# Performance work log

Hardware: AMD Instinct MI355X
Metric: run time of the kernel (lower is better)

The kernel has to match this reference:

```python
import jax, jax.numpy as jnp
import numpy as np

PAD_IDX = 0
EPS = 1e-5


def make_pos(L):
    # phrase[i, j] = j - i, i.e. row i is range(-i, L-i)
    phrase = (np.arange(L)[None, :] - np.arange(L)[:, None]).astype(np.float32)
    half = int(np.ceil(L / 2))
    freq = np.linspace(0.0, L, L, dtype=np.float32)[1:half]          # [F]
    pos = freq[:, None, None] * phrase[None] / L * 2.0 * np.pi       # [F, L, L]
    pos = np.concatenate([np.cos(pos), np.sin(pos)], axis=0)        # [2F, L, L]
    return jnp.asarray(np.transpose(pos, (1, 0, 2)))                # [L, P=2F, L]


def setup_inputs() -> dict:
    key = jax.random.key(0)
    ks = jax.random.split(key, 8)
    B, L, V, D, H = 2048, 64, 4096, 64, 8
    P = 2 * (int(np.ceil(L / 2)) - 1)  # 62
    inputs = jax.random.randint(ks[0], (B, L), 0, V)
    W_emb = jax.random.normal(ks[1], (V, D), jnp.float32) * 0.02
    W_emb = W_emb.at[PAD_IDX].set(0.0)  # padding_idx row is zero
    W_qkv = jax.random.normal(ks[2], (3 * H * D, D), jnp.float32) * 0.02
    W_pos = jax.random.normal(ks[3], (P, L), jnp.float32) * 0.02
    ln_g = jnp.ones((D,), jnp.float32)
    ln_b = jnp.zeros((D,), jnp.float32)
    W1 = jax.random.normal(ks[4], (64, H), jnp.float32) * 0.1
    b1 = jnp.zeros((64,), jnp.float32)
    W2 = jax.random.normal(ks[5], (32, 64), jnp.float32) * 0.1
    b2 = jnp.zeros((32,), jnp.float32)
    return dict(inputs=inputs, W_emb=W_emb, W_qkv=W_qkv, W_pos=W_pos,
                ln_g=ln_g, ln_b=ln_b, W1=W1, b1=b1, W2=W2, b2=b2,
                n_words=4, n_names=16)


def reference(inputs, W_emb, W_qkv, W_pos, ln_g, ln_b, W1, b1, W2, b2, n_words, n_names):
    B, L = inputs.shape
    V, D = W_emb.shape
    H = W_qkv.shape[0] // (3 * D)
    pos = make_pos(L)  # [L, P, L]
    P = pos.shape[1]

    # compute_qkv: per-char q/k/v tables, then gather per token.
    qkv = (W_emb @ W_qkv.T).reshape(V, 3 * H, D)
    q, k, v = qkv[:, :H], qkv[:, H:2 * H], qkv[:, 2 * H:]
    q_t = jnp.take(q, inputs, axis=0)  # [B, L, H, D]
    k_t = jnp.take(k, inputs, axis=0)
    v_t = jnp.take(v, inputs, axis=0)

    # Equivalent to gathering char_sim[h, ids, ids]: qkv is a per-token linear,
    # so q[ids] @ k[ids]^T == char_sim.index_select(1, ids).index_select(-1, ids).
    sim = jnp.einsum('blhd,bmhd->bhlm', q_t, k_t) / jnp.sqrt(jnp.float32(D))
    key_pad = (inputs == PAD_IDX)[:, None, None, :]
    sim = jnp.where(key_pad, jnp.float32(-1e9), sim)  # char_sim[:, :, pad_idx] = -1e9

    # positional bias: Linear(L->P) on clipped scores, contracted with pos basis.
    sim_clip = jnp.where(sim > -1e8, sim, jnp.float32(0.0))
    pos_w = jnp.einsum('bhlm,pm->bhlp', sim_clip, W_pos)        # [B, H, L, P]
    pos_bias = jnp.einsum('bhlp,lpm->bhlm', pos_w, pos) / P     # mean over P

    attn = jax.nn.softmax(sim + pos_bias, axis=-1)              # dropout p=0 -> id
    out = jnp.einsum('bhlm,bmhd->blhd', attn, v_t)              # [B, L, H, D]

    # sdpa LayerNorm over word_vec_d
    mu = out.mean(-1, keepdims=True)
    var = out.var(-1, keepdims=True)
    out = (out - mu) * jax.lax.rsqrt(var + EPS) * ln_g + ln_b

    # MLP over the head dimension: [B, L, D, H] -> [B, L, D, 32]
    ft = jnp.swapaxes(out, 2, 3)
    h1 = jax.nn.relu(jnp.einsum('bldh,oh->bldo', ft, W1) + b1)
    h2 = jnp.einsum('bldo,po->bldp', h1, W2) + b2
    char_ft = h2.reshape(B, L, -1)                              # [B, L, D*32]

    # masked mean pooling over chars -> word feature
    maskf = (inputs != PAD_IDX).astype(char_ft.dtype)
    word_ft = jnp.einsum('bl,blf->bf', maskf, char_ft) / maskf.sum(-1, keepdims=True)

    # equal-size splits: words -> names (mean) -> groups of names
    Fdim = word_ft.shape[-1]
    name_ft = word_ft.reshape(B // n_words, n_words, Fdim).mean(1)
    return name_ft.reshape(-1, n_names, Fdim)
```

## Files before the change

### kernel.cpp

```cpp
#include <hip/hip_runtime.h>
#include <hip/hip_bf16.h>


typedef __attribute__((ext_vector_type(8))) short short8;
typedef __attribute__((ext_vector_type(4))) float f32x4;

union FragU { uint4 u; short8 v; };

__device__ __forceinline__ unsigned short f2bf(float f) {
    union { float f; unsigned int i; } c; c.f = f;
    unsigned int i = c.i;
    unsigned int r = (i + 0x7fffu + ((i >> 16) & 1u)) >> 16;
    return (unsigned short)r;
}
__device__ __forceinline__ float asf(unsigned int u) {
    union { unsigned int i; float f; } c; c.i = u; return c.f;
}
__device__ __forceinline__ float bfsel(uint2 g, int i) {
    unsigned u = (i < 2) ? g.x : g.y;
    return asf((i & 1) ? (u & 0xffff0000u) : (u << 16));
}

__device__ __forceinline__ void packstore4(unsigned* rowptr, int c,
                                           float v0, float v1, float v2, float v3) {
    float p0 = __shfl_xor(v0, 1), p1 = __shfl_xor(v1, 1);
    float p2 = __shfl_xor(v2, 1), p3 = __shfl_xor(v3, 1);
    int odd = c & 1;
    unsigned a0 = odd ? ((unsigned)f2bf(p2) | ((unsigned)f2bf(v2) << 16))
                      : ((unsigned)f2bf(v0) | ((unsigned)f2bf(p0) << 16));
    unsigned a1 = odd ? ((unsigned)f2bf(p3) | ((unsigned)f2bf(v3) << 16))
                      : ((unsigned)f2bf(v1) | ((unsigned)f2bf(p1) << 16));
    int ba = (c >> 1) + (odd ? 16 : 0);
    rowptr[ba] = a0; rowptr[ba + 8] = a1;
}

__global__ __launch_bounds__(256) void k_qkv(const float* __restrict__ W_emb,
                                             const float* __restrict__ W_qkv,
                                             unsigned short* __restrict__ qkvb) {
    __shared__ float At[4096];
    __shared__ float Bt[4096];
    int t = threadIdx.x;
    int bt = blockIdx.x / 24, rt = blockIdx.x - bt * 24;
    int r = t >> 2, part = t & 3;
    const float4* esrc = (const float4*)(W_emb + (size_t)((bt << 6) + r) * 64 + part * 16);
    const float4* wsrc = (const float4*)(W_qkv + (size_t)((rt << 6) + r) * 64 + part * 16);
#pragma unroll
    for (int j = 0; j < 4; ++j) {
        float4 e4 = esrc[j], w4 = wsrc[j];
        int c0 = part * 16 + j * 4;
        At[(c0 + 0) * 64 + r] = e4.x; At[(c0 + 1) * 64 + r] = e4.y;
        At[(c0 + 2) * 64 + r] = e4.z; At[(c0 + 3) * 64 + r] = e4.w;
        Bt[(c0 + 0) * 64 + r] = w4.x; Bt[(c0 + 1) * 64 + r] = w4.y;
        Bt[(c0 + 2) * 64 + r] = w4.z; Bt[(c0 + 3) * 64 + r] = w4.w;
    }
    __syncthreads();
    int l0 = (t >> 4) << 2, m0 = (t & 15) << 2;
    float acc[4][4] = {};
#pragma unroll 4
    for (int k = 0; k < 64; ++k) {
        float4 a  = *(const float4*)(At + k * 64 + l0);
        float4 bb = *(const float4*)(Bt + k * 64 + m0);
        float aa[4] = {a.x, a.y, a.z, a.w};
        float bv[4] = {bb.x, bb.y, bb.z, bb.w};
#pragma unroll
        for (int i = 0; i < 4; ++i)
#pragma unroll
            for (int j = 0; j < 4; ++j)
                acc[i][j] = fmaf(aa[i], bv[j], acc[i][j]);
    }
#pragma unroll
    for (int i = 0; i < 4; ++i) {
        unsigned w0 = (unsigned)f2bf(acc[i][0]) | ((unsigned)f2bf(acc[i][1]) << 16);
        unsigned w1 = (unsigned)f2bf(acc[i][2]) | ((unsigned)f2bf(acc[i][3]) << 16);
        unsigned* dst = (unsigned*)(qkvb + (size_t)((bt << 6) + l0 + i) * 1536 + (rt << 6) + m0);
        dst[0] = w0; dst[1] = w1;
    }
}

__global__ void k_tab(const float* __restrict__ W_pos,
                      unsigned short* __restrict__ cst,
                      unsigned short* __restrict__ csl,
                      unsigned short* __restrict__ wpos) {
    int t = threadIdx.x;
    const float w = 6.283185307179586f / 63.0f;
    for (int e = t; e < 4096; e += 256) {
        int row = e >> 6, col = e & 63;
        {
            int j = col, x = row;
            float val = 0.0f;
            if (j < 31)       val = cosf(w * (float)(((j + 1) * x) % 63));
            else if (j >= 32 && j < 63) val = sinf(w * (float)(((j - 31) * x) % 63));
            cst[e] = f2bf(val);
        }
        {
            int j = row, x = col;
            float val = 0.0f;
            if (j < 31)       val = cosf(w * (float)(((j + 1) * x) % 63));
            else if (j >= 32 && j < 63) val = sinf(w * (float)(((j - 31) * x) % 63));
            csl[e] = f2bf(val);
        }
        {
            int j = row;
            float val = 0.0f;
            if (j < 31) val = W_pos[j * 64 + col];
            else if (j >= 32 && j < 63) val = W_pos[(j - 1) * 64 + col];
            wpos[e] = f2bf(val);
        }
    }
}

__global__ __launch_bounds__(128, 4) void k_attn(
    const int* __restrict__ inputs,
    const unsigned short* __restrict__ qkvb,
    const unsigned short* __restrict__ cstg,
    const unsigned short* __restrict__ cslg,
    const unsigned short* __restrict__ wposg,
    const float* __restrict__ ln_g,
    const float* __restrict__ ln_b,
    unsigned short* __restrict__ out_n)
{
    __shared__ __align__(16) unsigned int smem[4608];
    unsigned int* S0d = smem;
    unsigned int* S1d = smem + 2304;
    int t = threadIdx.x, w2 = t >> 6, lane = t & 63;
    int b = blockIdx.x >> 3, h = blockIdx.x & 7;
    const int* toks = inputs + b * 64;
    int r = lane & 15, q = lane >> 4, c = r;
    int tk = toks[lane];
    int mt0 = 2 * w2;

    int mk[4]; float gvv[4], bvv[4];
#pragma unroll
    for (int nt = 0; nt < 4; ++nt) {
        mk[nt] = (toks[16 * nt + c] == 0);
        gvv[nt] = ln_g[16 * nt + c];
        bvv[nt] = ln_b[16 * nt + c];
    }

    {
        const uint4* src = (const uint4*)(qkvb + (size_t)tk * 1536 + (w2 ? 512 : 0) + h * 64);
        uint4* dst = (uint4*)((w2 ? S1d : S0d) + lane * 36);
#pragma unroll
        for (int j = 0; j < 8; ++j) dst[j] = src[j];
    }
    __syncthreads();

    f32x4 sc[2][4], acc[2][4];
    const f32x4 zf = {0.f, 0.f, 0.f, 0.f};

#pragma unroll
    for (int u = 0; u < 2; ++u)
#pragma unroll
        for (int nt = 0; nt < 4; ++nt) sc[u][nt] = zf;
#pragma unroll
    for (int ks = 0; ks < 2; ++ks) {
        FragU Af[2], Bf[4];
#pragma unroll
        for (int u = 0; u < 2; ++u)
            Af[u].u = *(const uint4*)(S0d + (16 * (mt0 + u) + r) * 36 + 16 * ks + 4 * q);
#pragma unroll
        for (int nt = 0; nt < 4; ++nt)
            Bf[nt].u = *(const uint4*)(S1d + (16 * nt + r) * 36 + 16 * ks + 4 * q);
#pragma unroll
        for (int u = 0; u < 2; ++u)
#pragma unroll
            for (int nt = 0; nt < 4; ++nt)
                sc[u][nt] = __builtin_amdgcn_mfma_f32_16x16x32_bf16(Af[u].v, Bf[nt].v, sc[u][nt], 0, 0, 0);
    }
#pragma unroll
    for (int u = 0; u < 2; ++u) {
#pragma unroll
        for (int nt = 0; nt < 4; ++nt) {
            f32x4 vv = sc[u][nt];
#pragma unroll
            for (int i = 0; i < 4; ++i) vv[i] = mk[nt] ? 0.0f : vv[i] * 0.125f;
            sc[u][nt] = vv;
        }
#pragma unroll
        for (int i = 0; i < 4; ++i) {
            int l = 16 * (mt0 + u) + 4 * q + i;
            packstore4(S0d + l * 36, c, sc[u][0][i], sc[u][1][i], sc[u][2][i], sc[u][3][i]);
        }
    }
    __syncthreads();

#pragma unroll
    for (int u = 0; u < 2; ++u)
#pragma unroll
        for (int nt = 0; nt < 4; ++nt) acc[u][nt] = zf;
#pragma unroll
    for (int ks = 0; ks < 2; ++ks) {
        FragU Af[2], Bf[4];
#pragma unroll
        for (int u = 0; u < 2; ++u)
            Af[u].u = *(const uint4*)(S0d + (16 * (mt0 + u) + r) * 36 + 16 * ks + 4 * q);
#pragma unroll
        for (int nt = 0; nt < 4; ++nt)
            Bf[nt].u = *(const uint4*)(wposg + (16 * nt + r) * 64 + 32 * ks + 8 * q);
#pragma unroll
        for (int u = 0; u < 2; ++u)
#pragma unroll
            for (int nt = 0; nt < 4; ++nt)
                acc[u][nt] = __builtin_amdgcn_mfma_f32_16x16x32_bf16(Af[u].v, Bf[nt].v, acc[u][nt], 0, 0, 0);
    }
#pragma unroll
    for (int u = 0; u < 2; ++u) {
        int mt = mt0 + u;
        uint2 t00 = *(const uint2*)(cslg + (c) * 64 + 16 * mt + 4 * q);
        uint2 t01 = *(const uint2*)(cslg + (32 + c) * 64 + 16 * mt + 4 * q);
        uint2 t10 = *(const uint2*)(cslg + (16 + c) * 64 + 16 * mt + 4 * q);
        uint2 t11 = *(const uint2*)(cslg + (48 + c) * 64 + 16 * mt + 4 * q);
#pragma unroll
        for (int i = 0; i < 4; ++i) {
            int l = 16 * mt + 4 * q + i;
            float cv0 = bfsel(t00, i), sv0 = bfsel(t01, i);
            float cv1 = bfsel(t10, i), sv1 = bfsel(t11, i);
            float pc0 = acc[u][0][i], ps0 = acc[u][2][i];
            float pc1 = acc[u][1][i], ps1 = acc[u][3][i];
            float u0 = pc0 * cv0 - ps0 * sv0;
            float u1 = pc1 * cv1 - ps1 * sv1;
            float u2 = pc0 * sv0 + ps0 * cv0;
            float u3 = pc1 * sv1 + ps1 * cv1;
            packstore4(S1d + l * 36, c, u0, u1, u2, u3);
        }
    }

#pragma unroll
    for (int u = 0; u < 2; ++u)
#pragma unroll
        for (int nt = 0; nt < 4; ++nt) acc[u][nt] = zf;
#pragma unroll
    for (int ks = 0; ks < 2; ++ks) {
        FragU Af[2], Bf[4];
#pragma unroll
        for (int u = 0; u < 2; ++u)
            Af[u].u = *(const uint4*)(S1d + (16 * (mt0 + u) + r) * 36 + 16 * ks + 4 * q);
#pragma unroll
        for (int nt = 0; nt < 4; ++nt)
            Bf[nt].u = *(const uint4*)(cstg + (16 * nt + r) * 64 + 32 * ks + 8 * q);
#pragma unroll
        for (int u = 0; u < 2; ++u)
#pragma unroll
            for (int nt = 0; nt < 4; ++nt)
                acc[u][nt] = __builtin_amdgcn_mfma_f32_16x16x32_bf16(Af[u].v, Bf[nt].v, acc[u][nt], 0, 0, 0);
    }

    uint4 V4[4];
    {
        const uint4* vsrc = (const uint4*)(qkvb + (size_t)tk * 1536 + 1024 + h * 64 + 32 * w2);
#pragma unroll
        for (int j = 0; j < 4; ++j) V4[j] = vsrc[j];
    }

#pragma unroll
    for (int u = 0; u < 2; ++u)
#pragma unroll
        for (int i = 0; i < 4; ++i) {
            int l = 16 * (mt0 + u) + 4 * q + i;
            float e0 = mk[0] ? 0.f : __expf(fmaf(acc[u][0][i], 1.0f / 62.0f, sc[u][0][i]));
            float e1 = mk[1] ? 0.f : __expf(fmaf(acc[u][1][i], 1.0f / 62.0f, sc[u][1][i]));
            float e2 = mk[2] ? 0.f : __expf(fmaf(acc[u][2][i], 1.0f / 62.0f, sc[u][2][i]));
            float e3 = mk[3] ? 0.f : __expf(fmaf(acc[u][3][i], 1.0f / 62.0f, sc[u][3][i]));
            float s = e0 + e1 + e2 + e3;
            s += __shfl_xor(s, 1);
            s += __shfl_xor(s, 2);
            s += __shfl_xor(s, 4);
            s += __shfl_xor(s, 8);
            float inv = 1.0f / s;
            packstore4(S0d + l * 36, c, e0 * inv, e1 * inv, e2 * inv, e3 * inv);
        }

    {
        int odd = lane & 1;
        const unsigned* Vd = (const unsigned*)V4;
#pragma unroll
        for (int jj = 0; jj < 16; ++jj) {
            unsigned my = Vd[jj];
            unsigned pr = __shfl_xor(my, 1);
            unsigned val = odd ? ((pr >> 16) | (my & 0xffff0000u))
                               : ((my & 0xffffu) | (pr << 16));
            S1d[(32 * w2 + 2 * jj + odd) * 36 + (lane >> 1)] = val;
        }
    }
    __syncthreads();

#pragma unroll
    for (int u = 0; u < 2; ++u)
#pragma unroll
        for (int nt = 0; nt < 4; ++nt) acc[u][nt] = zf;
#pragma unroll
    for (int ks = 0; ks < 2; ++ks) {
        FragU Af[2], Bf[4];
#pragma unroll
        for (int u = 0; u < 2; ++u)
            Af[u].u = *(const uint4*)(S0d + (16 * (mt0 + u) + r) * 36 + 16 * ks + 4 * q);
#pragma unroll
        for (int nt = 0; nt < 4; ++nt)
            Bf[nt].u = *(const uint4*)(S1d + (16 * nt + r) * 36 + 16 * ks + 4 * q);
#pragma unroll
        for (int u = 0; u < 2; ++u)
#pragma unroll
            for (int nt = 0; nt < 4; ++nt)
                acc[u][nt] = __builtin_amdgcn_mfma_f32_16x16x32_bf16(Af[u].v, Bf[nt].v, acc[u][nt], 0, 0, 0);
    }
    {
        unsigned* outw = (unsigned*)out_n;
        size_t hb = ((size_t)b * 8 + h) * 64;
#pragma unroll
        for (int u = 0; u < 2; ++u)
#pragma unroll
            for (int i = 0; i < 4; ++i) {
                int l = 16 * (mt0 + u) + 4 * q + i;
                float v0 = acc[u][0][i], v1 = acc[u][1][i], v2 = acc[u][2][i], v3 = acc[u][3][i];
                float s1 = v0 + v1 + v2 + v3;
                float s2 = v0 * v0 + v1 * v1 + v2 * v2 + v3 * v3;
                s1 += __shfl_xor(s1, 1); s2 += __shfl_xor(s2, 1);
                s1 += __shfl_xor(s1, 2); s2 += __shfl_xor(s2, 2);
                s1 += __shfl_xor(s1, 4); s2 += __shfl_xor(s2, 4);
                s1 += __shfl_xor(s1, 8); s2 += __shfl_xor(s2, 8);
                float mu = s1 * (1.0f / 64.0f);
                float var = s2 * (1.0f / 64.0f) - mu * mu;
                float rstd = rsqrtf(var + 1e-5f);
                float y0 = (v0 - mu) * rstd * gvv[0] + bvv[0];
                float y1 = (v1 - mu) * rstd * gvv[1] + bvv[1];
                float y2 = (v2 - mu) * rstd * gvv[2] + bvv[2];
                float y3 = (v3 - mu) * rstd * gvv[3] + bvv[3];
                packstore4(outw + (hb + l) * 32, c, y0, y1, y2, y3);
            }
    }
}

__global__ __launch_bounds__(256) void k_mlp(const int* __restrict__ inputs,
                                             const unsigned short* __restrict__ out_n,
                                             const float* __restrict__ W1,
                                             const float* __restrict__ b1,
                                             float* __restrict__ gws) {
    __shared__ unsigned short XT[8320];
    __shared__ float wl[64];
    int t = threadIdx.x, w = t >> 6, lane = t & 63;
    int b = blockIdx.x;
    int ot = w >> 1, dt = w & 1;
    int kq = lane >> 4, n = lane & 15;

    if (t < 64) {
        int tok = inputs[b * 64 + t];
        unsigned long long bal = __ballot(tok != 0);
        int cnt = __popcll(bal);
        if (cnt < 1) cnt = 1;
        wl[t] = (tok != 0) ? 1.0f / (float)cnt : 0.0f;
    }

    FragU Wf[2];
    float b1v[2];
#pragma unroll
    for (int om = 0; om < 2; ++om) {
        int o = 32 * ot + 16 * om + n;
        b1v[om] = b1[o];
        if (kq == 0) {
            const float4* wsrc = (const float4*)(W1 + o * 8);
            float4 wa = wsrc[0], wb = wsrc[1];
            Wf[om].u.x = (unsigned)f2bf(wa.x) | ((unsigned)f2bf(wa.y) << 16);
            Wf[om].u.y = (unsigned)f2bf(wa.z) | ((unsigned)f2bf(wa.w) << 16);
            Wf[om].u.z = (unsigned)f2bf(wb.x) | ((unsigned)f2bf(wb.y) << 16);
            Wf[om].u.w = (unsigned)f2bf(wb.z) | ((unsigned)f2bf(wb.w) << 16);
        } else {
            Wf[om].u = make_uint4(0, 0, 0, 0);
        }
    }

    f32x4 racc[2][2];
    const f32x4 zf = {0.f, 0.f, 0.f, 0.f};
#pragma unroll
    for (int dm = 0; dm < 2; ++dm)
#pragma unroll
        for (int om = 0; om < 2; ++om) racc[dm][om] = zf;

    int lh = t & 7;
    int lr = (t >> 3) & 15;
    int half = t >> 7;

    for (int cc = 0; cc < 4; ++cc) {
        __syncthreads();
        {
            const unsigned short* src = out_n + (size_t)b * 32768 + lh * 4096
                                        + (16 * cc + lr) * 64 + half * 32;
            unsigned short* dst = XT + lr * 520 + lh;
#pragma unroll
            for (int j = 0; j < 4; ++j) {
                uint4 u = ((const uint4*)src)[j];
                int d0 = half * 32 + j * 8;
                dst[(d0 + 0) * 8] = (unsigned short)(u.x & 0xffffu);
                dst[(d0 + 1) * 8] = (unsigned short)(u.x >> 16);
                dst[(d0 + 2) * 8] = (unsigned short)(u.y & 0xffffu);
                dst[(d0 + 3) * 8] = (unsigned short)(u.y >> 16);
                dst[(d0 + 4) * 8] = (unsigned short)(u.z & 0xffffu);
                dst[(d0 + 5) * 8] = (unsigned short)(u.z >> 16);
                dst[(d0 + 6) * 8] = (unsigned short)(u.w & 0xffffu);
                dst[(d0 + 7) * 8] = (unsigned short)(u.w >> 16);
            }
        }
        __syncthreads();
#pragma unroll 4
        for (int l = 0; l < 16; ++l) {
            FragU Xf[2];
#pragma unroll
            for (int dm = 0; dm < 2; ++dm) {
                if (kq == 0)
                    Xf[dm].u = *(const uint4*)(XT + l * 520 + (32 * dt + 16 * dm + n) * 8);
                else
                    Xf[dm].u = make_uint4(0, 0, 0, 0);
            }
            float wv = wl[16 * cc + l];
#pragma unroll
            for (int dm = 0; dm < 2; ++dm)
#pragma unroll
                for (int om = 0; om < 2; ++om) {
                    f32x4 C = __builtin_amdgcn_mfma_f32_16x16x32_bf16(Xf[dm].v, Wf[om].v, zf, 0, 0, 0);
#pragma unroll
                    for (int i = 0; i < 4; ++i)
                        racc[dm][om][i] = fmaf(wv, fmaxf(C[i] + b1v[om], 0.0f), racc[dm][om][i]);
                }
        }
    }
    float* gb = gws + (size_t)b * 4096;
#pragma unroll
    for (int dm = 0; dm < 2; ++dm)
#pragma unroll
        for (int om = 0; om < 2; ++om) {
            int o = 32 * ot + 16 * om + n;
#pragma unroll
            for (int i = 0; i < 4; ++i) {
                int d = 32 * dt + 16 * dm + 4 * kq + i;
                gb[d * 64 + o] = racc[dm][om][i];
            }
        }
}

__global__ __launch_bounds__(256) void k_final(const float* __restrict__ gws,
                                               const float* __restrict__ W2,
                                               const float* __restrict__ b2,
                                               float* __restrict__ out) {
    __shared__ float gbar[4096];
    __shared__ float w2s[32 * 68];
    __shared__ float b2s[32];
    int t = threadIdx.x;
    int n = blockIdx.x;
    for (int e = t; e < 4096; e += 256) {
        size_t base = (size_t)(4 * n) * 4096 + e;
        gbar[e] = 0.25f * (gws[base] + gws[base + 4096] + gws[base + 8192] + gws[base + 12288]);
    }
    for (int e = t; e < 2048; e += 256) {
        int p = e >> 6, o = e & 63;
        w2s[p * 68 + o] = W2[e];
    }
    if (t < 32) b2s[t] = b2[t];
    __syncthreads();
#pragma unroll
    for (int jj = 0; jj < 8; ++jj) {
        int f = jj * 256 + t;
        int d = f >> 5, p = f & 31;
        float acc = b2s[p];
        for (int o4 = 0; o4 < 16; ++o4) {
            float4 gvv = *(const float4*)(gbar + d * 64 + o4 * 4);
            float4 wv = *(const float4*)(w2s + p * 68 + o4 * 4);
            acc = fmaf(gvv.x, wv.x, acc);
            acc = fmaf(gvv.y, wv.y, acc);
            acc = fmaf(gvv.z, wv.z, acc);
            acc = fmaf(gvv.w, wv.w, acc);
        }
        out[(size_t)n * 2048 + f] = acc;
    }
}

extern "C" void kernel_launch(void* const* d_in, const int* in_sizes, int n_in,
                              void* d_out, int out_size, void* d_ws, size_t ws_size,
                              hipStream_t stream) {
    const int*   inputs = (const int*)d_in[0];
    const float* W_emb  = (const float*)d_in[1];
    const float* W_qkv  = (const float*)d_in[2];
    const float* W_pos  = (const float*)d_in[3];
    const float* ln_g   = (const float*)d_in[4];
    const float* ln_b   = (const float*)d_in[5];
    const float* W1     = (const float*)d_in[6];
    const float* b1     = (const float*)d_in[7];
    const float* W2     = (const float*)d_in[8];
    const float* b2     = (const float*)d_in[9];
    float* out = (float*)d_out;

    unsigned short* qkvb = (unsigned short*)d_ws;
    unsigned short* cst  = qkvb + 6291456;
    unsigned short* csl  = cst + 4096;
    unsigned short* wpos = csl + 4096;
    float* gws = (float*)(wpos + 4096);
    unsigned short* out_n = (unsigned short*)(gws + 8388608);

    hipLaunchKernelGGL(k_qkv,   dim3(64 * 24), dim3(256), 0, stream, W_emb, W_qkv, qkvb);
    hipLaunchKernelGGL(k_tab,   dim3(1),       dim3(256), 0, stream, W_pos, cst, csl, wpos);
    hipLaunchKernelGGL(k_attn,  dim3(16384),   dim3(128), 0, stream,
                       inputs, qkvb, cst, csl, wpos, ln_g, ln_b, out_n);
    hipLaunchKernelGGL(k_mlp,   dim3(2048),    dim3(256), 0, stream, inputs, out_n, W1, b1, gws);
    hipLaunchKernelGGL(k_final, dim3(512),     dim3(256), 0, stream, gws, W2, b2, out);
}
```

Before: 401.9 us.

## Swizzle attention LDS layout, use hardware bf16 packing and fast math, skip pad chars

Replaces the padded 36-word LDS row stride with a 32-word stride and an XOR swizzle, which shrinks shared memory and keeps MFMA fragment reads free of bank conflicts. Float-to-bf16 packing now uses the v_cvt_pk_bf16_f32 instruction, and softmax uses exp2 with the log2(e) factor folded into the score scale, plus hardware rcp and rsq. The positional cos/sin table is stored as fp32 so the per-element bf16 unpacking goes away, and LayerNorm is rewritten as fmas. In the MLP, the bias is folded into the MFMA through a constant-one input lane, padded characters are skipped via a ballot mask, and the mean division moves to the final store. Fast-math intrinsics and the bias rounded to bf16 slightly change numerics.

```diff
diff --git a/kernel.cpp b/kernel.cpp
--- a/kernel.cpp
+++ b/kernel.cpp
@@ -13,25 +13,22 @@
     unsigned int r = (i + 0x7fffu + ((i >> 16) & 1u)) >> 16;
     return (unsigned short)r;
 }
-__device__ __forceinline__ float asf(unsigned int u) {
-    union { unsigned int i; float f; } c; c.i = u; return c.f;
-}
-__device__ __forceinline__ float bfsel(uint2 g, int i) {
-    unsigned u = (i < 2) ? g.x : g.y;
-    return asf((i & 1) ? (u & 0xffff0000u) : (u << 16));
-}
-
-__device__ __forceinline__ void packstore4(unsigned* rowptr, int c,
+
+__device__ __forceinline__ unsigned cvtpk(float lo, float hi) {
+    unsigned r;
+    asm("v_cvt_pk_bf16_f32 %0, %1, %2" : "=v"(r) : "v"(lo), "v"(hi));
+    return r;
+}
+
+__device__ __forceinline__ void packstore4(unsigned* rowbase, int X, int c,
                                            float v0, float v1, float v2, float v3) {
     float p0 = __shfl_xor(v0, 1), p1 = __shfl_xor(v1, 1);
     float p2 = __shfl_xor(v2, 1), p3 = __shfl_xor(v3, 1);
     int odd = c & 1;
-    unsigned a0 = odd ? ((unsigned)f2bf(p2) | ((unsigned)f2bf(v2) << 16))
-                      : ((unsigned)f2bf(v0) | ((unsigned)f2bf(p0) << 16));
-    unsigned a1 = odd ? ((unsigned)f2bf(p3) | ((unsigned)f2bf(v3) << 16))
-                      : ((unsigned)f2bf(v1) | ((unsigned)f2bf(p1) << 16));
-    int ba = (c >> 1) + (odd ? 16 : 0);
-    rowptr[ba] = a0; rowptr[ba + 8] = a1;
+    unsigned a0 = odd ? cvtpk(p2, v2) : cvtpk(v0, p0);
+    unsigned a1 = odd ? cvtpk(p3, v3) : cvtpk(v1, p1);
+    int ba = (((c >> 1) + (odd ? 16 : 0)) ^ X);
+    rowbase[ba] = a0; rowbase[ba ^ 8] = a1;
 }
 
 __global__ __launch_bounds__(256) void k_qkv(const float* __restrict__ W_emb,
@@ -70,8 +67,8 @@
     }
 #pragma unroll
     for (int i = 0; i < 4; ++i) {
-        unsigned w0 = (unsigned)f2bf(acc[i][0]) | ((unsigned)f2bf(acc[i][1]) << 16);
-        unsigned w1 = (unsigned)f2bf(acc[i][2]) | ((unsigned)f2bf(acc[i][3]) << 16);
+        unsigned w0 = cvtpk(acc[i][0], acc[i][1]);
+        unsigned w1 = cvtpk(acc[i][2], acc[i][3]);
         unsigned* dst = (unsigned*)(qkvb + (size_t)((bt << 6) + l0 + i) * 1536 + (rt << 6) + m0);
         dst[0] = w0; dst[1] = w1;
     }
@@ -79,7 +76,7 @@
 
 __global__ void k_tab(const float* __restrict__ W_pos,
                       unsigned short* __restrict__ cst,
-                      unsigned short* __restrict__ csl,
+                      float* __restrict__ cslf,
                       unsigned short* __restrict__ wpos) {
     int t = threadIdx.x;
     const float w = 6.283185307179586f / 63.0f;
@@ -97,7 +94,7 @@
             float val = 0.0f;
             if (j < 31)       val = cosf(w * (float)(((j + 1) * x) % 63));
             else if (j >= 32 && j < 63) val = sinf(w * (float)(((j - 31) * x) % 63));
-            csl[e] = f2bf(val);
+            cslf[e] = val;
         }
         {
             int j = row;
@@ -113,21 +110,24 @@
     const int* __restrict__ inputs,
     const unsigned short* __restrict__ qkvb,
     const unsigned short* __restrict__ cstg,
-    const unsigned short* __restrict__ cslg,
+    const float* __restrict__ cslf,
     const unsigned short* __restrict__ wposg,
     const float* __restrict__ ln_g,
     const float* __restrict__ ln_b,
     unsigned short* __restrict__ out_n)
 {
-    __shared__ __align__(16) unsigned int smem[4608];
+    __shared__ __align__(16) unsigned int smem[4096];
     unsigned int* S0d = smem;
-    unsigned int* S1d = smem + 2304;
+    unsigned int* S1d = smem + 2048;
     int t = threadIdx.x, w2 = t >> 6, lane = t & 63;
     int b = blockIdx.x >> 3, h = blockIdx.x & 7;
     const int* toks = inputs + b * 64;
     int r = lane & 15, q = lane >> 4, c = r;
+    int rx = (r & 7) << 2;
     int tk = toks[lane];
     int mt0 = 2 * w2;
+    const float LAM = 0.18033688f;
+    const float INV62 = 1.0f / 62.0f;
 
     int mk[4]; float gvv[4], bvv[4];
 #pragma unroll
@@ -139,9 +139,10 @@
 
     {
         const uint4* src = (const uint4*)(qkvb + (size_t)tk * 1536 + (w2 ? 512 : 0) + h * 64);
-        uint4* dst = (uint4*)((w2 ? S1d : S0d) + lane * 36);
-#pragma unroll
-        for (int j = 0; j < 8; ++j) dst[j] = src[j];
+        uint4* dst = (uint4*)((w2 ? S1d : S0d) + (lane << 5));
+        int sx = lane & 7;
+#pragma unroll
+        for (int j = 0; j < 8; ++j) dst[j ^ sx] = src[j];
     }
     __syncthreads();
 
@@ -157,10 +158,10 @@
         FragU Af[2], Bf[4];
 #pragma unroll
         for (int u = 0; u < 2; ++u)
-            Af[u].u = *(const uint4*)(S0d + (16 * (mt0 + u) + r) * 36 + 16 * ks + 4 * q);
+            Af[u].u = *(const uint4*)(S0d + ((16 * (mt0 + u) + r) << 5) + ((16 * ks + 4 * q) ^ rx));
 #pragma unroll
         for (int nt = 0; nt < 4; ++nt)
-            Bf[nt].u = *(const uint4*)(S1d + (16 * nt + r) * 36 + 16 * ks + 4 * q);
+            Bf[nt].u = *(const uint4*)(S1d + ((16 * nt + r) << 5) + ((16 * ks + 4 * q) ^ rx));
 #pragma unroll
         for (int u = 0; u < 2; ++u)
 #pragma unroll
@@ -173,13 +174,13 @@
         for (int nt = 0; nt < 4; ++nt) {
             f32x4 vv = sc[u][nt];
 #pragma unroll
-            for (int i = 0; i < 4; ++i) vv[i] = mk[nt] ? 0.0f : vv[i] * 0.125f;
+            for (int i = 0; i < 4; ++i) vv[i] = mk[nt] ? 0.0f : vv[i] * LAM;
             sc[u][nt] = vv;
         }
 #pragma unroll
         for (int i = 0; i < 4; ++i) {
             int l = 16 * (mt0 + u) + 4 * q + i;
-            packstore4(S0d + l * 36, c, sc[u][0][i], sc[u][1][i], sc[u][2][i], sc[u][3][i]);
+            packstore4(S0d + (l << 5), (l & 7) << 2, c, sc[u][0][i], sc[u][1][i], sc[u][2][i], sc[u][3][i]);
         }
     }
     __syncthreads();
@@ -193,7 +194,7 @@
         FragU Af[2], Bf[4];
 #pragma unroll
         for (int u = 0; u < 2; ++u)
-            Af[u].u = *(const uint4*)(S0d + (16 * (mt0 + u) + r) * 36 + 16 * ks + 4 * q);
+            Af[u].u = *(const uint4*)(S0d + ((16 * (mt0 + u) + r) << 5) + ((16 * ks + 4 * q) ^ rx));
 #pragma unroll
         for (int nt = 0; nt < 4; ++nt)
             Bf[nt].u = *(const uint4*)(wposg + (16 * nt + r) * 64 + 32 * ks + 8 * q);
@@ -206,22 +207,20 @@
 #pragma unroll
     for (int u = 0; u < 2; ++u) {
         int mt = mt0 + u;
-        uint2 t00 = *(const uint2*)(cslg + (c) * 64 + 16 * mt + 4 * q);
-        uint2 t01 = *(const uint2*)(cslg + (32 + c) * 64 + 16 * mt + 4 * q);
-        uint2 t10 = *(const uint2*)(cslg + (16 + c) * 64 + 16 * mt + 4 * q);
-        uint2 t11 = *(const uint2*)(cslg + (48 + c) * 64 + 16 * mt + 4 * q);
+        f32x4 cc0 = *(const f32x4*)(cslf + (c) * 64 + 16 * mt + 4 * q);
+        f32x4 ss0 = *(const f32x4*)(cslf + (32 + c) * 64 + 16 * mt + 4 * q);
+        f32x4 cc1 = *(const f32x4*)(cslf + (16 + c) * 64 + 16 * mt + 4 * q);
+        f32x4 ss1 = *(const f32x4*)(cslf + (48 + c) * 64 + 16 * mt + 4 * q);
 #pragma unroll
         for (int i = 0; i < 4; ++i) {
             int l = 16 * mt + 4 * q + i;
-            float cv0 = bfsel(t00, i), sv0 = bfsel(t01, i);
-            float cv1 = bfsel(t10, i), sv1 = bfsel(t11, i);
             float pc0 = acc[u][0][i], ps0 = acc[u][2][i];
             float pc1 = acc[u][1][i], ps1 = acc[u][3][i];
-            float u0 = pc0 * cv0 - ps0 * sv0;
-            float u1 = pc1 * cv1 - ps1 * sv1;
-            float u2 = pc0 * sv0 + ps0 * cv0;
-            float u3 = pc1 * sv1 + ps1 * cv1;
-            packstore4(S1d + l * 36, c, u0, u1, u2, u3);
+            float u0 = pc0 * cc0[i] - ps0 * ss0[i];
+            float u1 = pc1 * cc1[i] - ps1 * ss1[i];
+            float u2 = pc0 * ss0[i] + ps0 * cc0[i];
+            float u3 = pc1 * ss1[i] + ps1 * cc1[i];
+            packstore4(S1d + (l << 5), (l & 7) << 2, c, u0, u1, u2, u3);
         }
     }
 
@@ -234,7 +233,7 @@
         FragU Af[2], Bf[4];
 #pragma unroll
         for (int u = 0; u < 2; ++u)
-            Af[u].u = *(const uint4*)(S1d + (16 * (mt0 + u) + r) * 36 + 16 * ks + 4 * q);
+            Af[u].u = *(const uint4*)(S1d + ((16 * (mt0 + u) + r) << 5) + ((16 * ks + 4 * q) ^ rx));
 #pragma unroll
         for (int nt = 0; nt < 4; ++nt)
             Bf[nt].u = *(const uint4*)(cstg + (16 * nt + r) * 64 + 32 * ks + 8 * q);
@@ -257,17 +256,17 @@
 #pragma unroll
         for (int i = 0; i < 4; ++i) {
             int l = 16 * (mt0 + u) + 4 * q + i;
-            float e0 = mk[0] ? 0.f : __expf(fmaf(acc[u][0][i], 1.0f / 62.0f, sc[u][0][i]));
-            float e1 = mk[1] ? 0.f : __expf(fmaf(acc[u][1][i], 1.0f / 62.0f, sc[u][1][i]));
-            float e2 = mk[2] ? 0.f : __expf(fmaf(acc[u][2][i], 1.0f / 62.0f, sc[u][2][i]));
-            float e3 = mk[3] ? 0.f : __expf(fmaf(acc[u][3][i], 1.0f / 62.0f, sc[u][3][i]));
+            float e0 = mk[0] ? 0.f : __builtin_amdgcn_exp2f(fmaf(acc[u][0][i], INV62, sc[u][0][i]));
+            float e1 = mk[1] ? 0.f : __builtin_amdgcn_exp2f(fmaf(acc[u][1][i], INV62, sc[u][1][i]));
+            float e2 = mk[2] ? 0.f : __builtin_amdgcn_exp2f(fmaf(acc[u][2][i], INV62, sc[u][2][i]));
+            float e3 = mk[3] ? 0.f : __builtin_amdgcn_exp2f(fmaf(acc[u][3][i], INV62, sc[u][3][i]));
             float s = e0 + e1 + e2 + e3;
             s += __shfl_xor(s, 1);
             s += __shfl_xor(s, 2);
             s += __shfl_xor(s, 4);
             s += __shfl_xor(s, 8);
-            float inv = 1.0f / s;
-            packstore4(S0d + l * 36, c, e0 * inv, e1 * inv, e2 * inv, e3 * inv);
+            float inv = __builtin_amdgcn_rcpf(s);
+            packstore4(S0d + (l << 5), (l & 7) << 2, c, e0 * inv, e1 * inv, e2 * inv, e3 * inv);
         }
 
     {
@@ -279,7 +278,8 @@
             unsigned pr = __shfl_xor(my, 1);
             unsigned val = odd ? ((pr >> 16) | (my & 0xffff0000u))
                                : ((my & 0xffffu) | (pr << 16));
-            S1d[(32 * w2 + 2 * jj + odd) * 36 + (lane >> 1)] = val;
+            int row = 32 * w2 + 2 * jj + odd;
+            S1d[(row << 5) + ((lane >> 1) ^ ((row & 7) << 2))] = val;
         }
     }
     __syncthreads();
@@ -293,10 +293,10 @@
         FragU Af[2], Bf[4];
 #pragma unroll
         for (int u = 0; u < 2; ++u)
-            Af[u].u = *(const uint4*)(S0d + (16 * (mt0 + u) + r) * 36 + 16 * ks + 4 * q);
+            Af[u].u = *(const uint4*)(S0d + ((16 * (mt0 + u) + r) << 5) + ((16 * ks + 4 * q) ^ rx));
 #pragma unroll
         for (int nt = 0; nt < 4; ++nt)
-            Bf[nt].u = *(const uint4*)(S1d + (16 * nt + r) * 36 + 16 * ks + 4 * q);
+            Bf[nt].u = *(const uint4*)(S1d + ((16 * nt + r) << 5) + ((16 * ks + 4 * q) ^ rx));
 #pragma unroll
         for (int u = 0; u < 2; ++u)
 #pragma unroll
@@ -320,12 +320,13 @@
                 s1 += __shfl_xor(s1, 8); s2 += __shfl_xor(s2, 8);
                 float mu = s1 * (1.0f / 64.0f);
                 float var = s2 * (1.0f / 64.0f) - mu * mu;
-                float rstd = rsqrtf(var + 1e-5f);
-                float y0 = (v0 - mu) * rstd * gvv[0] + bvv[0];
-                float y1 = (v1 - mu) * rstd * gvv[1] + bvv[1];
-                float y2 = (v2 - mu) * rstd * gvv[2] + bvv[2];
-                float y3 = (v3 - mu) * rstd * gvv[3] + bvv[3];
-                packstore4(outw + (hb + l) * 32, c, y0, y1, y2, y3);
+                float rstd = __builtin_amdgcn_rsqf(var + 1e-5f);
+                float cmu = -mu * rstd;
+                float y0 = fmaf(fmaf(v0, rstd, cmu), gvv[0], bvv[0]);
+                float y1 = fmaf(fmaf(v1, rstd, cmu), gvv[1], bvv[1]);
+                float y2 = fmaf(fmaf(v2, rstd, cmu), gvv[2], bvv[2]);
+                float y3 = fmaf(fmaf(v3, rstd, cmu), gvv[3], bvv[3]);
+                packstore4(outw + (hb + l) * 32, 0, c, y0, y1, y2, y3);
             }
     }
 }
@@ -336,7 +337,8 @@
                                              const float* __restrict__ b1,
                                              float* __restrict__ gws) {
     __shared__ unsigned short XT[8320];
-    __shared__ float wl[64];
+    __shared__ unsigned long long vmask_s;
+    __shared__ float invcnt_s;
     int t = threadIdx.x, w = t >> 6, lane = t & 63;
     int b = blockIdx.x;
     int ot = w >> 1, dt = w & 1;
@@ -345,24 +347,27 @@
     if (t < 64) {
         int tok = inputs[b * 64 + t];
         unsigned long long bal = __ballot(tok != 0);
-        int cnt = __popcll(bal);
-        if (cnt < 1) cnt = 1;
-        wl[t] = (tok != 0) ? 1.0f / (float)cnt : 0.0f;
+        if (t == 0) {
+            int cnt = __popcll(bal);
+            if (cnt < 1) cnt = 1;
+            vmask_s = bal;
+            invcnt_s = 1.0f / (float)cnt;
+        }
     }
 
     FragU Wf[2];
-    float b1v[2];
 #pragma unroll
     for (int om = 0; om < 2; ++om) {
         int o = 32 * ot + 16 * om + n;
-        b1v[om] = b1[o];
         if (kq == 0) {
             const float4* wsrc = (const float4*)(W1 + o * 8);
             float4 wa = wsrc[0], wb = wsrc[1];
-            Wf[om].u.x = (unsigned)f2bf(wa.x) | ((unsigned)f2bf(wa.y) << 16);
-            Wf[om].u.y = (unsigned)f2bf(wa.z) | ((unsigned)f2bf(wa.w) << 16);
-            Wf[om].u.z = (unsigned)f2bf(wb.x) | ((unsigned)f2bf(wb.y) << 16);
-            Wf[om].u.w = (unsigned)f2bf(wb.z) | ((unsigned)f2bf(wb.w) << 16);
+            Wf[om].u.x = cvtpk(wa.x, wa.y);
+            Wf[om].u.y = cvtpk(wa.z, wa.w);
+            Wf[om].u.z = cvtpk(wb.x, wb.y);
+            Wf[om].u.w = cvtpk(wb.z, wb.w);
+        } else if (kq == 1) {
+            Wf[om].u = make_uint4((unsigned)f2bf(b1[o]), 0, 0, 0);
         } else {
             Wf[om].u = make_uint4(0, 0, 0, 0);
         }
@@ -378,6 +383,10 @@
     int lh = t & 7;
     int lr = (t >> 3) & 15;
     int half = t >> 7;
+
+    __syncthreads();
+    unsigned long long vmask = vmask_s;
+    float invcnt = invcnt_s;
 
     for (int cc = 0; cc < 4; ++cc) {
         __syncthreads();
@@ -402,15 +411,17 @@
         __syncthreads();
 #pragma unroll 4
         for (int l = 0; l < 16; ++l) {
+            if (!((vmask >> (16 * cc + l)) & 1ull)) continue;
             FragU Xf[2];
 #pragma unroll
             for (int dm = 0; dm < 2; ++dm) {
                 if (kq == 0)
                     Xf[dm].u = *(const uint4*)(XT + l * 520 + (32 * dt + 16 * dm + n) * 8);
+                else if (kq == 1)
+                    Xf[dm].u = make_uint4(0x3F80u, 0, 0, 0);
                 else
                     Xf[dm].u = make_uint4(0, 0, 0, 0);
             }
-            float wv = wl[16 * cc + l];
 #pragma unroll
             for (int dm = 0; dm < 2; ++dm)
 #pragma unroll
@@ -418,7 +429,7 @@
                     f32x4 C = __builtin_amdgcn_mfma_f32_16x16x32_bf16(Xf[dm].v, Wf[om].v, zf, 0, 0, 0);
 #pragma unroll
                     for (int i = 0; i < 4; ++i)
-                        racc[dm][om][i] = fmaf(wv, fmaxf(C[i] + b1v[om], 0.0f), racc[dm][om][i]);
+                        racc[dm][om][i] += fmaxf(C[i], 0.0f);
                 }
         }
     }
@@ -431,7 +442,7 @@
 #pragma unroll
             for (int i = 0; i < 4; ++i) {
                 int d = 32 * dt + 16 * dm + 4 * kq + i;
-                gb[d * 64 + o] = racc[dm][om][i];
+                gb[d * 64 + o] = racc[dm][om][i] * invcnt;
             }
         }
 }
@@ -489,15 +500,15 @@
 
     unsigned short* qkvb = (unsigned short*)d_ws;
     unsigned short* cst  = qkvb + 6291456;
-    unsigned short* csl  = cst + 4096;
-    unsigned short* wpos = csl + 4096;
-    float* gws = (float*)(wpos + 4096);
+    unsigned short* wpos = cst + 4096;
+    float* cslf = (float*)(wpos + 4096);
+    float* gws  = cslf + 4096;
     unsigned short* out_n = (unsigned short*)(gws + 8388608);
 
     hipLaunchKernelGGL(k_qkv,   dim3(64 * 24), dim3(256), 0, stream, W_emb, W_qkv, qkvb);
-    hipLaunchKernelGGL(k_tab,   dim3(1),       dim3(256), 0, stream, W_pos, cst, csl, wpos);
+    hipLaunchKernelGGL(k_tab,   dim3(1),       dim3(256), 0, stream, W_pos, cst, cslf, wpos);
     hipLaunchKernelGGL(k_attn,  dim3(16384),   dim3(128), 0, stream,
-                       inputs, qkvb, cst, csl, wpos, ln_g, ln_b, out_n);
+                       inputs, qkvb, cst, cslf, wpos, ln_g, ln_b, out_n);
     hipLaunchKernelGGL(k_mlp,   dim3(2048),    dim3(256), 0, stream, inputs, out_n, W1, b1, gws);
     hipLaunchKernelGGL(k_final, dim3(512),     dim3(256), 0, stream, gws, W2, b2, out);
 }
```

New measurement: 433.9 us. 8.0% more time.
